# Optimization experiments

Hardware: AMD Instinct MI355X
Metric: run time of the kernel (lower is better)

The kernel has to match this reference:

```python
import jax, jax.numpy as jnp
import numpy as np

N_NODES = 50000
N_EDGES = 800000
IN_FEATS = 128
N_HIDDEN = 128
N_CLASSES = 47
LN_EPS = 1e-5


def _sage_conv(h, src, dst, w_self, w_neigh, b):
    # DGL SAGEConv 'mean': out = h_dst @ W_self + mean_neigh(h_src) @ W_neigh + b
    msg = h[src]  # [E, d] gather
    agg = jax.ops.segment_sum(msg, dst, num_segments=N_NODES)
    deg = jax.ops.segment_sum(jnp.ones((src.shape[0],), h.dtype), dst, num_segments=N_NODES)
    h_neigh = agg / jnp.maximum(deg, 1.0)[:, None]  # zero-degree nodes -> 0
    return h @ w_self + h_neigh @ w_neigh + b


def _layer_norm(h, gamma, beta):
    mu = jnp.mean(h, axis=-1, keepdims=True)
    var = jnp.mean(jnp.square(h - mu), axis=-1, keepdims=True)
    return (h - mu) * jax.lax.rsqrt(var + LN_EPS) * gamma + beta


def setup_inputs() -> dict:
    key = jax.random.key(0)
    ks = jax.random.split(key, 12)
    s = 0.05
    inp = {
        "x": jax.random.normal(ks[0], (N_NODES, IN_FEATS), jnp.float32),
        "src": jax.random.randint(ks[1], (N_EDGES,), 0, N_NODES, jnp.int32),
        "dst": jax.random.randint(ks[2], (N_EDGES,), 0, N_NODES, jnp.int32),
        # layer 0
        "w_self0": jax.random.normal(ks[3], (IN_FEATS, N_HIDDEN), jnp.float32) * s,
        "w_neigh0": jax.random.normal(ks[4], (IN_FEATS, N_HIDDEN), jnp.float32) * s,
        "b0": jnp.zeros((N_HIDDEN,), jnp.float32),
        "g0": jnp.ones((N_HIDDEN,), jnp.float32),
        "be0": jnp.zeros((N_HIDDEN,), jnp.float32),
        # layer 1
        "w_self1": jax.random.normal(ks[5], (N_HIDDEN, N_HIDDEN), jnp.float32) * s,
        "w_neigh1": jax.random.normal(ks[6], (N_HIDDEN, N_HIDDEN), jnp.float32) * s,
        "b1": jnp.zeros((N_HIDDEN,), jnp.float32),
        "g1": jnp.ones((N_HIDDEN,), jnp.float32),
        "be1": jnp.zeros((N_HIDDEN,), jnp.float32),
        # layer 2 (output)
        "w_self2": jax.random.normal(ks[7], (N_HIDDEN, N_CLASSES), jnp.float32) * s,
        "w_neigh2": jax.random.normal(ks[8], (N_HIDDEN, N_CLASSES), jnp.float32) * s,
        "b2": jnp.zeros((N_CLASSES,), jnp.float32),
    }
    return inp


def reference(x, src, dst,
              w_self0, w_neigh0, b0, g0, be0,
              w_self1, w_neigh1, b1, g1, be1,
              w_self2, w_neigh2, b2):
    h = _sage_conv(x, src, dst, w_self0, w_neigh0, b0)
    h = jax.nn.relu(_layer_norm(h, g0, be0))
    h = _sage_conv(h, src, dst, w_self1, w_neigh1, b1)
    h = jax.nn.relu(_layer_norm(h, g1, be1))
    h = _sage_conv(h, src, dst, w_self2, w_neigh2, b2)
    return h
```

## Files before the change

kernel.cpp:

```cpp
#include <hip/hip_runtime.h>

#define NN 50000
#define NE 800000
#define D 128
#define NCLS 47
#define ZPAD 64
#define LN_EPS 1e-5f

__global__ void k_count(const int* __restrict__ dst, int* __restrict__ counts) {
  int i = blockIdx.x * blockDim.x + threadIdx.x;
  if (i < NE) atomicAdd(&counts[dst[i]], 1);
}

__global__ void k_scan1(const int* __restrict__ counts, int* __restrict__ excl,
                        int* __restrict__ bsum) {
  __shared__ int tmp[256];
  int t = threadIdx.x, i = blockIdx.x * 256 + t;
  int v = (i < NN) ? counts[i] : 0;
  tmp[t] = v;
  __syncthreads();
  for (int off = 1; off < 256; off <<= 1) {
    int u = (t >= off) ? tmp[t - off] : 0;
    __syncthreads();
    tmp[t] += u;
    __syncthreads();
  }
  if (i < NN) excl[i] = tmp[t] - v;
  if (t == 255) bsum[blockIdx.x] = tmp[255];
}

__global__ void k_scan2(int* __restrict__ bsum, int nb) {
  __shared__ int tmp[256];
  int t = threadIdx.x;
  int v = (t < nb) ? bsum[t] : 0;
  tmp[t] = v;
  __syncthreads();
  for (int off = 1; off < 256; off <<= 1) {
    int u = (t >= off) ? tmp[t - off] : 0;
    __syncthreads();
    tmp[t] += u;
    __syncthreads();
  }
  if (t < nb) bsum[t] = tmp[t] - v;
}

__global__ void k_scan3(int* __restrict__ indptr, const int* __restrict__ bsum,
                        int* __restrict__ cursor) {
  int i = blockIdx.x * 256 + threadIdx.x;
  if (i < NN) {
    int v = indptr[i] + bsum[i >> 8];
    indptr[i] = v;
    cursor[i] = v;
  }
  if (i == 0) indptr[NN] = NE;
}

__global__ void k_scatter(const int* __restrict__ src, const int* __restrict__ dst,
                          int* __restrict__ cursor, int* __restrict__ esrc) {
  int i = blockIdx.x * blockDim.x + threadIdx.x;
  if (i < NE) {
    int d = dst[i];
    int pos = atomicAdd(&cursor[d], 1);
    esrc[pos] = src[i];
  }
}

__global__ __launch_bounds__(64) void k_agg(const float* __restrict__ feat,
                                            const int* __restrict__ indptr,
                                            const int* __restrict__ esrc,
                                            float* __restrict__ out) {
  int w = blockIdx.x;
  int lane = threadIdx.x;
  if (w >= NN) return;
  int beg = indptr[w], end = indptr[w + 1];
  float a0 = 0.f, a1 = 0.f;
  int e = beg;
  for (; e + 15 < end; e += 16) {
    int idx[16];
#pragma unroll
    for (int j = 0; j < 16; ++j) idx[j] = esrc[e + j];
    float2 v[16];
#pragma unroll
    for (int j = 0; j < 16; ++j)
      v[j] = *(const float2*)(feat + (size_t)idx[j] * D + lane * 2);
#pragma unroll
    for (int j = 0; j < 16; ++j) { a0 += v[j].x; a1 += v[j].y; }
  }
  for (; e + 3 < end; e += 4) {
    int i0 = esrc[e], i1 = esrc[e + 1], i2 = esrc[e + 2], i3 = esrc[e + 3];
    float2 v0 = *(const float2*)(feat + (size_t)i0 * D + lane * 2);
    float2 v1 = *(const float2*)(feat + (size_t)i1 * D + lane * 2);
    float2 v2 = *(const float2*)(feat + (size_t)i2 * D + lane * 2);
    float2 v3 = *(const float2*)(feat + (size_t)i3 * D + lane * 2);
    a0 += v0.x + v1.x + v2.x + v3.x;
    a1 += v0.y + v1.y + v2.y + v3.y;
  }
  for (; e < end; ++e) {
    float2 v0 = *(const float2*)(feat + (size_t)esrc[e] * D + lane * 2);
    a0 += v0.x;
    a1 += v0.y;
  }
  float inv = 1.0f / fmaxf((float)(end - beg), 1.0f);
  float2 o;
  o.x = a0 * inv;
  o.y = a1 * inv;
  *(float2*)(out + (size_t)w * D + lane * 2) = o;
}

__global__ __launch_bounds__(256, 4) void k_gemm_ln(
    const float* __restrict__ h, const float* __restrict__ hn,
    const float* __restrict__ ws, const float* __restrict__ wn,
    const float* __restrict__ b, const float* __restrict__ g,
    const float* __restrict__ be, float* __restrict__ out) {
  __shared__ float lds[32][256];
  int tid = threadIdx.x;
  int row0 = blockIdx.x * 32;
  for (int i = tid; i < 32 * 64; i += 256) {
    int r = i >> 6, q = i & 63;
    int row = row0 + r;
    float4 v = make_float4(0.f, 0.f, 0.f, 0.f);
    if (row < NN) {
      const float* p = (q < 32) ? (h + (size_t)row * D + q * 4)
                                : (hn + (size_t)row * D + (q - 32) * 4);
      v = *(const float4*)p;
    }
    *(float4*)&lds[r][q * 4] = v;
  }
  __syncthreads();

  int wv = tid >> 6, lane = tid & 63;
  int rbase = wv * 8;
  float acc0[8], acc1[8];
#pragma unroll
  for (int r = 0; r < 8; ++r) { acc0[r] = 0.f; acc1[r] = 0.f; }

  float cw[8], nw[8];
#pragma unroll
  for (int j = 0; j < 4; ++j) {
    cw[2 * j]     = ws[j * 128 + lane];
    cw[2 * j + 1] = ws[j * 128 + lane + 64];
  }
#pragma unroll 2
  for (int c = 0; c < 64; ++c) {
    int cn = (c + 1 < 64) ? c + 1 : 63;
    const float* np = ((cn & 32) ? wn : ws) + (cn & 31) * 512;
    float4 hv[8];
#pragma unroll
    for (int r = 0; r < 8; ++r) hv[r] = *(const float4*)&lds[rbase + r][c * 4];
#pragma unroll
    for (int j = 0; j < 4; ++j) {
      nw[2 * j]     = np[j * 128 + lane];
      nw[2 * j + 1] = np[j * 128 + lane + 64];
    }
#pragma unroll
    for (int r = 0; r < 8; ++r) {
      acc0[r] = fmaf(hv[r].x, cw[0], acc0[r]);
      acc1[r] = fmaf(hv[r].x, cw[1], acc1[r]);
      acc0[r] = fmaf(hv[r].y, cw[2], acc0[r]);
      acc1[r] = fmaf(hv[r].y, cw[3], acc1[r]);
      acc0[r] = fmaf(hv[r].z, cw[4], acc0[r]);
      acc1[r] = fmaf(hv[r].z, cw[5], acc1[r]);
      acc0[r] = fmaf(hv[r].w, cw[6], acc0[r]);
      acc1[r] = fmaf(hv[r].w, cw[7], acc1[r]);
    }
#pragma unroll
    for (int j = 0; j < 8; ++j) cw[j] = nw[j];
  }

  float bj0 = b[lane], bj1 = b[lane + 64];
  float gj0 = g[lane], gj1 = g[lane + 64];
  float ej0 = be[lane], ej1 = be[lane + 64];
#pragma unroll
  for (int r = 0; r < 8; ++r) {
    float v0 = acc0[r] + bj0, v1 = acc1[r] + bj1;
    float s = v0 + v1, q2 = v0 * v0 + v1 * v1;
#pragma unroll
    for (int off = 1; off < 64; off <<= 1) {
      s += __shfl_xor(s, off, 64);
      q2 += __shfl_xor(q2, off, 64);
    }
    float mu = s * (1.0f / 128.0f);
    float var = q2 * (1.0f / 128.0f) - mu * mu;
    float rs = rsqrtf(var + LN_EPS);
    float o0 = fmaxf((v0 - mu) * rs * gj0 + ej0, 0.f);
    float o1 = fmaxf((v1 - mu) * rs * gj1 + ej1, 0.f);
    int row = row0 + rbase + r;
    if (row < NN) {
      out[(size_t)row * D + lane] = o0;
      out[(size_t)row * D + lane + 64] = o1;
    }
  }
}

__global__ __launch_bounds__(256, 4) void k_gemm_proj2(
    const float* __restrict__ h, const float* __restrict__ ws,
    const float* __restrict__ wn, const float* __restrict__ b,
    float* __restrict__ s2p, float* __restrict__ z2) {
  __shared__ float lds[32][128];
  int tid = threadIdx.x;
  int row0 = blockIdx.x * 32;
  for (int i = tid; i < 32 * 32; i += 256) {
    int r = i >> 5, q = i & 31;
    int row = row0 + r;
    float4 v = make_float4(0.f, 0.f, 0.f, 0.f);
    if (row < NN) v = *(const float4*)(h + (size_t)row * D + q * 4);
    *(float4*)&lds[r][q * 4] = v;
  }
  __syncthreads();

  int wv = tid >> 6, lane = tid & 63;
  int rbase = wv * 8;
  bool act = lane < NCLS;
  float accS[8], accZ[8];
#pragma unroll
  for (int r = 0; r < 8; ++r) { accS[r] = 0.f; accZ[r] = 0.f; }

  float cw[8], nw[8];
#pragma unroll
  for (int j = 0; j < 4; ++j) {
    cw[j]     = act ? ws[j * NCLS + lane] : 0.f;
    cw[4 + j] = act ? wn[j * NCLS + lane] : 0.f;
  }
#pragma unroll 2
  for (int c = 0; c < 32; ++c) {
    int cn = (c + 1 < 32) ? c + 1 : 31;
    float4 hv[8];
#pragma unroll
    for (int r = 0; r < 8; ++r) hv[r] = *(const float4*)&lds[rbase + r][c * 4];
#pragma unroll
    for (int j = 0; j < 4; ++j) {
      nw[j]     = act ? ws[(cn * 4 + j) * NCLS + lane] : 0.f;
      nw[4 + j] = act ? wn[(cn * 4 + j) * NCLS + lane] : 0.f;
    }
#pragma unroll
    for (int r = 0; r < 8; ++r) {
      accS[r] = fmaf(hv[r].x, cw[0], accS[r]);
      accZ[r] = fmaf(hv[r].x, cw[4], accZ[r]);
      accS[r] = fmaf(hv[r].y, cw[1], accS[r]);
      accZ[r] = fmaf(hv[r].y, cw[5], accZ[r]);
      accS[r] = fmaf(hv[r].z, cw[2], accS[r]);
      accZ[r] = fmaf(hv[r].z, cw[6], accZ[r]);
      accS[r] = fmaf(hv[r].w, cw[3], accS[r]);
      accZ[r] = fmaf(hv[r].w, cw[7], accZ[r]);
    }
#pragma unroll
    for (int j = 0; j < 8; ++j) cw[j] = nw[j];
  }

  float bj = act ? b[lane] : 0.f;
#pragma unroll
  for (int r = 0; r < 8; ++r) {
    int row = row0 + rbase + r;
    if (row < NN) {
      z2[(size_t)row * ZPAD + lane] = act ? accZ[r] : 0.f;
      s2p[(size_t)row * ZPAD + lane] = accS[r] + bj;
    }
  }
}

__global__ __launch_bounds__(64) void k_agg2(const float* __restrict__ z2,
                                             const float* __restrict__ s2p,
                                             const int* __restrict__ indptr,
                                             const int* __restrict__ esrc,
                                             float* __restrict__ out) {
  int w = blockIdx.x;
  int lane = threadIdx.x;
  if (w >= NN) return;
  int beg = indptr[w], end = indptr[w + 1];
  float a = 0.f;
  int e = beg;
  for (; e + 15 < end; e += 16) {
    int idx[16];
#pragma unroll
    for (int j = 0; j < 16; ++j) idx[j] = esrc[e + j];
    float v[16];
#pragma unroll
    for (int j = 0; j < 16; ++j) v[j] = z2[(size_t)idx[j] * ZPAD + lane];
#pragma unroll
    for (int j = 0; j < 16; ++j) a += v[j];
  }
  for (; e + 3 < end; e += 4) {
    int i0 = esrc[e], i1 = esrc[e + 1], i2 = esrc[e + 2], i3 = esrc[e + 3];
    a += z2[(size_t)i0 * ZPAD + lane] + z2[(size_t)i1 * ZPAD + lane] +
         z2[(size_t)i2 * ZPAD + lane] + z2[(size_t)i3 * ZPAD + lane];
  }
  for (; e < end; ++e) a += z2[(size_t)esrc[e] * ZPAD + lane];
  float inv = 1.0f / fmaxf((float)(end - beg), 1.0f);
  if (lane < NCLS)
    out[(size_t)w * NCLS + lane] = s2p[(size_t)w * ZPAD + lane] + a * inv;
}

extern "C" void kernel_launch(void* const* d_in, const int* in_sizes, int n_in,
                              void* d_out, int out_size, void* d_ws, size_t ws_size,
                              hipStream_t stream) {
  (void)in_sizes; (void)n_in; (void)out_size; (void)ws_size;
  const float* x       = (const float*)d_in[0];
  const int*   src     = (const int*)d_in[1];
  const int*   dst     = (const int*)d_in[2];
  const float* w_self0 = (const float*)d_in[3];
  const float* w_nei0  = (const float*)d_in[4];
  const float* b0      = (const float*)d_in[5];
  const float* g0      = (const float*)d_in[6];
  const float* be0     = (const float*)d_in[7];
  const float* w_self1 = (const float*)d_in[8];
  const float* w_nei1  = (const float*)d_in[9];
  const float* b1      = (const float*)d_in[10];
  const float* g1      = (const float*)d_in[11];
  const float* be1     = (const float*)d_in[12];
  const float* w_self2 = (const float*)d_in[13];
  const float* w_nei2  = (const float*)d_in[14];
  const float* b2      = (const float*)d_in[15];
  float* outp = (float*)d_out;

  char* ws = (char*)d_ws;
  size_t off = 0;
  auto alloc = [&](size_t bytes) -> void* {
    off = (off + 255) & ~(size_t)255;
    void* p = ws + off;
    off += bytes;
    return p;
  };
  int*   counts = (int*)alloc(NN * sizeof(int));
  int*   indptr = (int*)alloc((NN + 1) * sizeof(int));
  int*   cursor = (int*)alloc(NN * sizeof(int));
  int*   bsum   = (int*)alloc(256 * sizeof(int));
  int*   esrc   = (int*)alloc(NE * sizeof(int));
  float* hn     = (float*)alloc((size_t)NN * D * sizeof(float));
  float* h1     = (float*)alloc((size_t)NN * D * sizeof(float));
  float* h2     = (float*)alloc((size_t)NN * D * sizeof(float));
  float* z2  = hn;
  float* s2p = h1;

  const int nbScan = (NN + 255) / 256;

  hipMemsetAsync(counts, 0, NN * sizeof(int), stream);
  k_count<<<(NE + 255) / 256, 256, 0, stream>>>(dst, counts);
  k_scan1<<<nbScan, 256, 0, stream>>>(counts, indptr, bsum);
  k_scan2<<<1, 256, 0, stream>>>(bsum, nbScan);
  k_scan3<<<nbScan, 256, 0, stream>>>(indptr, bsum, cursor);
  k_scatter<<<(NE + 255) / 256, 256, 0, stream>>>(src, dst, cursor, esrc);

  const int gemmBlocks = (NN + 31) / 32;

  k_agg<<<NN, 64, 0, stream>>>(x, indptr, esrc, hn);
  k_gemm_ln<<<gemmBlocks, 256, 0, stream>>>(x, hn, w_self0, w_nei0, b0, g0, be0, h1);
  k_agg<<<NN, 64, 0, stream>>>(h1, indptr, esrc, hn);
  k_gemm_ln<<<gemmBlocks, 256, 0, stream>>>(h1, hn, w_self1, w_nei1, b1, g1, be1, h2);
  k_gemm_proj2<<<gemmBlocks, 256, 0, stream>>>(h2, w_self2, w_nei2, b2, s2p, z2);
  k_agg2<<<NN, 64, 0, stream>>>(z2, s2p, indptr, esrc, outp);
}
```

Measured before the change: 488.7 us.

## Fuse neighbor mean aggregation into the GEMM+LayerNorm kernel for layers 0 and 1

The separate k_agg kernel is removed. Each 256-thread GEMM block now gathers and averages neighbor features for its 32 rows directly into the LDS half that previously held the hn tile, which avoids writing and re-reading the 50000x128 intermediate and saves a launch per layer. In exchange, each wave processes its 8 nodes one after another inside a block limited by launch_bounds(256,4). That gives less memory-level parallelism for the irregular gather than one 64-thread block per node, and the GEMM cannot start until the slowest node's gather finishes.

Result: no change. 481.5 us (-1.5%).

```diff
diff --git a/kernel.cpp b/kernel.cpp
--- a/kernel.cpp
+++ b/kernel.cpp
@@ -65,71 +65,66 @@
   }
 }
 
-__global__ __launch_bounds__(64) void k_agg(const float* __restrict__ feat,
-                                            const int* __restrict__ indptr,
-                                            const int* __restrict__ esrc,
-                                            float* __restrict__ out) {
-  int w = blockIdx.x;
-  int lane = threadIdx.x;
-  if (w >= NN) return;
-  int beg = indptr[w], end = indptr[w + 1];
-  float a0 = 0.f, a1 = 0.f;
-  int e = beg;
-  for (; e + 15 < end; e += 16) {
-    int idx[16];
-#pragma unroll
-    for (int j = 0; j < 16; ++j) idx[j] = esrc[e + j];
-    float2 v[16];
-#pragma unroll
-    for (int j = 0; j < 16; ++j)
-      v[j] = *(const float2*)(feat + (size_t)idx[j] * D + lane * 2);
-#pragma unroll
-    for (int j = 0; j < 16; ++j) { a0 += v[j].x; a1 += v[j].y; }
-  }
-  for (; e + 3 < end; e += 4) {
-    int i0 = esrc[e], i1 = esrc[e + 1], i2 = esrc[e + 2], i3 = esrc[e + 3];
-    float2 v0 = *(const float2*)(feat + (size_t)i0 * D + lane * 2);
-    float2 v1 = *(const float2*)(feat + (size_t)i1 * D + lane * 2);
-    float2 v2 = *(const float2*)(feat + (size_t)i2 * D + lane * 2);
-    float2 v3 = *(const float2*)(feat + (size_t)i3 * D + lane * 2);
-    a0 += v0.x + v1.x + v2.x + v3.x;
-    a1 += v0.y + v1.y + v2.y + v3.y;
-  }
-  for (; e < end; ++e) {
-    float2 v0 = *(const float2*)(feat + (size_t)esrc[e] * D + lane * 2);
-    a0 += v0.x;
-    a1 += v0.y;
-  }
-  float inv = 1.0f / fmaxf((float)(end - beg), 1.0f);
-  float2 o;
-  o.x = a0 * inv;
-  o.y = a1 * inv;
-  *(float2*)(out + (size_t)w * D + lane * 2) = o;
-}
-
-__global__ __launch_bounds__(256, 4) void k_gemm_ln(
-    const float* __restrict__ h, const float* __restrict__ hn,
+__global__ __launch_bounds__(256, 4) void k_sage_ln(
+    const float* __restrict__ h, const int* __restrict__ indptr,
+    const int* __restrict__ esrc,
     const float* __restrict__ ws, const float* __restrict__ wn,
     const float* __restrict__ b, const float* __restrict__ g,
     const float* __restrict__ be, float* __restrict__ out) {
   __shared__ float lds[32][256];
   int tid = threadIdx.x;
   int row0 = blockIdx.x * 32;
-  for (int i = tid; i < 32 * 64; i += 256) {
-    int r = i >> 6, q = i & 63;
+  int wv = tid >> 6, lane = tid & 63;
+  int rbase = wv * 8;
+
+  for (int i = tid; i < 32 * 32; i += 256) {
+    int r = i >> 5, q = i & 31;
     int row = row0 + r;
     float4 v = make_float4(0.f, 0.f, 0.f, 0.f);
-    if (row < NN) {
-      const float* p = (q < 32) ? (h + (size_t)row * D + q * 4)
-                                : (hn + (size_t)row * D + (q - 32) * 4);
-      v = *(const float4*)p;
-    }
+    if (row < NN) v = *(const float4*)(h + (size_t)row * D + q * 4);
     *(float4*)&lds[r][q * 4] = v;
   }
+
+  for (int i = 0; i < 8; ++i) {
+    int node = row0 + rbase + i;
+    float a0 = 0.f, a1 = 0.f;
+    if (node < NN) {
+      int beg = indptr[node], end = indptr[node + 1];
+      int e = beg;
+      for (; e + 15 < end; e += 16) {
+        int idx[16];
+#pragma unroll
+        for (int j = 0; j < 16; ++j) idx[j] = esrc[e + j];
+        float2 v[16];
+#pragma unroll
+        for (int j = 0; j < 16; ++j)
+          v[j] = *(const float2*)(h + (size_t)idx[j] * D + lane * 2);
+#pragma unroll
+        for (int j = 0; j < 16; ++j) { a0 += v[j].x; a1 += v[j].y; }
+      }
+      for (; e + 3 < end; e += 4) {
+        int i0 = esrc[e], i1 = esrc[e + 1], i2 = esrc[e + 2], i3 = esrc[e + 3];
+        float2 v0 = *(const float2*)(h + (size_t)i0 * D + lane * 2);
+        float2 v1 = *(const float2*)(h + (size_t)i1 * D + lane * 2);
+        float2 v2 = *(const float2*)(h + (size_t)i2 * D + lane * 2);
+        float2 v3 = *(const float2*)(h + (size_t)i3 * D + lane * 2);
+        a0 += v0.x + v1.x + v2.x + v3.x;
+        a1 += v0.y + v1.y + v2.y + v3.y;
+      }
+      for (; e < end; ++e) {
+        float2 v0 = *(const float2*)(h + (size_t)esrc[e] * D + lane * 2);
+        a0 += v0.x;
+        a1 += v0.y;
+      }
+      float inv = 1.0f / fmaxf((float)(end - beg), 1.0f);
+      a0 *= inv;
+      a1 *= inv;
+    }
+    float2 o; o.x = a0; o.y = a1;
+    *(float2*)&lds[rbase + i][128 + lane * 2] = o;
+  }
   __syncthreads();
 
-  int wv = tid >> 6, lane = tid & 63;
-  int rbase = wv * 8;
   float acc0[8], acc1[8];
 #pragma unroll
   for (int r = 0; r < 8; ++r) { acc0[r] = 0.f; acc1[r] = 0.f; }
@@ -325,10 +320,9 @@
   int*   cursor = (int*)alloc(NN * sizeof(int));
   int*   bsum   = (int*)alloc(256 * sizeof(int));
   int*   esrc   = (int*)alloc(NE * sizeof(int));
-  float* hn     = (float*)alloc((size_t)NN * D * sizeof(float));
   float* h1     = (float*)alloc((size_t)NN * D * sizeof(float));
   float* h2     = (float*)alloc((size_t)NN * D * sizeof(float));
-  float* z2  = hn;
+  float* z2     = (float*)alloc((size_t)NN * ZPAD * sizeof(float));
   float* s2p = h1;
 
   const int nbScan = (NN + 255) / 256;
@@ -342,10 +336,10 @@
 
   const int gemmBlocks = (NN + 31) / 32;
 
-  k_agg<<<NN, 64, 0, stream>>>(x, indptr, esrc, hn);
-  k_gemm_ln<<<gemmBlocks, 256, 0, stream>>>(x, hn, w_self0, w_nei0, b0, g0, be0, h1);
-  k_agg<<<NN, 64, 0, stream>>>(h1, indptr, esrc, hn);
-  k_gemm_ln<<<gemmBlocks, 256, 0, stream>>>(h1, hn, w_self1, w_nei1, b1, g1, be1, h2);
+  k_sage_ln<<<gemmBlocks, 256, 0, stream>>>(x, indptr, esrc, w_self0, w_nei0,
+                                            b0, g0, be0, h1);
+  k_sage_ln<<<gemmBlocks, 256, 0, stream>>>(h1, indptr, esrc, w_self1, w_nei1,
+                                            b1, g1, be1, h2);
   k_gemm_proj2<<<gemmBlocks, 256, 0, stream>>>(h2, w_self2, w_nei2, b2, s2p, z2);
   k_agg2<<<NN, 64, 0, stream>>>(z2, s2p, indptr, esrc, outp);
 }
```
